# Kernel optimization log

Measured on AMD Instinct MI355X. Metric: run time of the kernel, lower is better.

## Reference

```python
import jax, jax.numpy as jnp
import numpy as np
from jax import lax

# module constants (from init_kwargs)
IN_CH = 128
OUT_CH = 128
CTX = 128
KS = 3
STRIDE = 1
PAD = 1
GROUPS = 1
ATT_GROUPS = 1
K = 4
TEMP = 30.0  # T_max, used as the fixed temperature at init


def setup_inputs() -> dict:
    key = jax.random.key(0)
    k1, k2, k3, k4, k5 = jax.random.split(key, 5)
    b, f, t = 16, 64, 256
    x = jax.random.normal(k1, (b, IN_CH, f, t), dtype=jnp.float32)
    g = jax.random.normal(k2, (1, b, CTX), dtype=jnp.float32)
    # Dense(k*att_groups) params (kaiming-normal kernel, zero bias)
    fan_in = CTX
    dense_kernel = jax.random.normal(k3, (CTX, K * ATT_GROUPS), dtype=jnp.float32) * np.sqrt(2.0 / fan_in)
    dense_bias = jnp.zeros((K * ATT_GROUPS,), dtype=jnp.float32)
    # kernel bank: (k, out, in//groups, ks, ks) -> swapaxes(1,2) -> flatten to (1, att_groups, k, -1)
    flat = OUT_CH * (IN_CH // GROUPS) * KS * KS // ATT_GROUPS
    weight = jax.random.normal(k4, (1, ATT_GROUPS, K, flat), dtype=jnp.float32) * np.sqrt(2.0 / flat)
    return {"x": x, "g": g, "dense_kernel": dense_kernel, "dense_bias": dense_bias, "weight": weight}


def reference(x, g, dense_kernel, dense_bias, weight):
    b, c, f, t = x.shape
    g_c = g[0].reshape(b, -1)                                  # [b, ctx]
    residuals = (g_c @ dense_kernel + dense_bias).reshape(b, ATT_GROUPS, 1, -1)  # [b, ag, 1, k]
    attention = jax.nn.softmax(residuals / TEMP, axis=-1)      # [b, ag, 1, k]
    # per-sample kernel aggregation: [b, ag, 1, k] @ [1, ag, k, D] -> [b, ag, 1, D]
    agg = (attention @ weight).swapaxes(1, 2)                  # [b, 1, ag, D]
    agg = agg.reshape(b * OUT_CH, IN_CH // GROUPS, KS, KS)
    # batch-as-groups grouped conv
    out = lax.conv_general_dilated(
        x.reshape(1, b * c, f, t), agg,
        window_strides=(STRIDE, STRIDE),
        padding=[(PAD, PAD), (PAD, PAD)],
        dimension_numbers=("NCHW", "OIHW", "NCHW"),
        feature_group_count=b * GROUPS,
    )
    return out.reshape(b, OUT_CH, out.shape[-2], out.shape[-1])
```

## Files before the change

kernel.cpp:

```cpp
#include <hip/hip_runtime.h>
#include <stdint.h>

#define NB 16
#define NC 128
#define NOC 128
#define NF 64
#define NT 256
#define NCTX 128
#define NTAPS 9
#define NFLAT 147456
#define TEMPR 30.0f

#define ICP 40
#define XCOLS 258
#define SX_ELEMS (3*XCOLS*ICP)
#define SW_ELEMS (NTAPS*NOC*ICP)

typedef float f32x4 __attribute__((ext_vector_type(4)));
typedef __bf16 bf16x8 __attribute__((ext_vector_type(8)));
typedef unsigned int u32x4 __attribute__((ext_vector_type(4)));

__device__ __forceinline__ unsigned short f2bf(float f) {
    union { float f; unsigned u; } v; v.f = f;
    unsigned r = v.u + 0x7fffu + ((v.u >> 16) & 1u);
    return (unsigned short)(r >> 16);
}

__global__ void attn_kernel(const float* __restrict__ g,
                            const float* __restrict__ dk,
                            const float* __restrict__ bias,
                            float* __restrict__ att) {
    int b = threadIdx.x;
    if (b >= NB) return;
    float r0 = bias[0], r1 = bias[1], r2 = bias[2], r3 = bias[3];
    const float* gb = g + b * NCTX;
    for (int c = 0; c < NCTX; ++c) {
        float gv = gb[c];
        r0 += gv * dk[c*4+0];
        r1 += gv * dk[c*4+1];
        r2 += gv * dk[c*4+2];
        r3 += gv * dk[c*4+3];
    }
    r0 *= (1.0f/TEMPR); r1 *= (1.0f/TEMPR); r2 *= (1.0f/TEMPR); r3 *= (1.0f/TEMPR);
    float mx = fmaxf(fmaxf(r0, r1), fmaxf(r2, r3));
    float e0 = expf(r0-mx), e1 = expf(r1-mx), e2 = expf(r2-mx), e3 = expf(r3-mx);
    float s = e0+e1+e2+e3;
    att[b*4+0] = e0/s; att[b*4+1] = e1/s; att[b*4+2] = e2/s; att[b*4+3] = e3/s;
}

__global__ void agg_kernel(const float* __restrict__ w,
                           const float* __restrict__ att,
                           unsigned short* __restrict__ wb) {
    int idx = blockIdx.x * 256 + threadIdx.x;
    int ic = idx & 127;
    int oc = (idx >> 7) & 127;
    int b  = idx >> 14;
    float a0 = att[b*4+0], a1 = att[b*4+1], a2 = att[b*4+2], a3 = att[b*4+3];
    int d0 = (oc*NC + ic) * NTAPS;
    #pragma unroll
    for (int tap = 0; tap < NTAPS; ++tap) {
        float s = a0 * w[0*NFLAT + d0 + tap]
                + a1 * w[1*NFLAT + d0 + tap]
                + a2 * w[2*NFLAT + d0 + tap]
                + a3 * w[3*NFLAT + d0 + tap];
        wb[((b*NTAPS + tap)*NOC + oc)*NC + ic] = f2bf(s);
    }
}

__global__ __launch_bounds__(512) void conv_kernel(
        const float* __restrict__ x,
        const unsigned short* __restrict__ wb,
        float* __restrict__ out) {
    __shared__ unsigned short sx[SX_ELEMS];
    __shared__ unsigned short sw[SW_ELEMS];

    const int p  = blockIdx.x;
    const int lg = (p & 7) * 128 + (p >> 3);
    const int b  = lg >> 6;
    const int y  = lg & 63;

    const int tid  = threadIdx.x;
    const int lane = tid & 63;
    const int wid  = tid >> 6;
    const int wpix = wid & 3;
    const int woc  = wid >> 2;
    const int l15  = lane & 15;
    const int l4   = lane >> 4;

    f32x4 acc[4][4];
    #pragma unroll
    for (int m = 0; m < 4; ++m)
        #pragma unroll
        for (int n = 0; n < 4; ++n)
            acc[m][n] = (f32x4){0.f, 0.f, 0.f, 0.f};

    const float* xb = x + (b * NC) * (NF * NT);
    const unsigned short* wbb = wb + b * (NTAPS * NOC * NC);

    for (int c4 = 0; c4 < 4; ++c4) {
        const int ic0 = c4 * 32;
        __syncthreads();

        #pragma unroll
        for (int j = 0; j < 6; ++j) {
            int w_  = tid + j * 512;
            int qlo = w_ & 3;
            int i2  = (w_ >> 2) & 15;
            int qhi = (w_ >> 6) & 15;
            int r   = w_ >> 10;
            int q   = qhi * 4 + qlo;
            int iy  = y - 1 + r;
            f32x4 v0 = (f32x4){0.f,0.f,0.f,0.f};
            f32x4 v1 = v0;
            if ((unsigned)iy < (unsigned)NF) {
                const float* src = xb + ((ic0 + 2*i2) * NF + iy) * NT + q * 4;
                v0 = *(const f32x4*)src;
                v1 = *(const f32x4*)(src + NF * NT);
            }
            unsigned short* dst = sx + (r * XCOLS + q*4 + 1) * ICP + 2*i2;
            #pragma unroll
            for (int jj = 0; jj < 4; ++jj) {
                unsigned pk = (unsigned)f2bf(v0[jj]) | ((unsigned)f2bf(v1[jj]) << 16);
                *(unsigned*)(dst + jj * ICP) = pk;
            }
        }
        if (tid < 96) {
            int i2 = tid & 15;
            int rr = tid >> 4;
            int r  = rr % 3;
            int c  = (rr / 3) ? (XCOLS - 1) : 0;
            *(unsigned*)(sx + (r * XCOLS + c) * ICP + 2*i2) = 0u;
        }

        #pragma unroll
        for (int j = 0; j < 9; ++j) {
            int w_  = tid + j * 512;
            int row = w_ >> 2;
            int q4  = w_ & 3;
            u32x4 d = *(const u32x4*)(wbb + row * NC + ic0 + q4 * 8);
            *(u32x4*)(sw + row * ICP + q4 * 8) = d;
        }
        __syncthreads();

        const unsigned short* swp = sw + (woc * 64 + l15) * ICP + l4 * 8;
        const unsigned short* sxp = sx + (wpix * 64 + l15) * ICP + l4 * 8;
        #pragma unroll
        for (int ky = 0; ky < 3; ++ky) {
            #pragma unroll
            for (int kx = 0; kx < 3; ++kx) {
                const int tap = ky * 3 + kx;
                bf16x8 af[4], bfv[4];
                #pragma unroll
                for (int m = 0; m < 4; ++m)
                    af[m] = *(const bf16x8*)(swp + (tap * NOC + m * 16) * ICP);
                #pragma unroll
                for (int n = 0; n < 4; ++n)
                    bfv[n] = *(const bf16x8*)(sxp + (ky * XCOLS + kx + n * 16) * ICP);
                #pragma unroll
                for (int m = 0; m < 4; ++m)
                    #pragma unroll
                    for (int n = 0; n < 4; ++n)
                        acc[m][n] = __builtin_amdgcn_mfma_f32_16x16x32_bf16(
                            af[m], bfv[n], acc[m][n], 0, 0, 0);
            }
        }
    }

    #pragma unroll
    for (int m = 0; m < 4; ++m) {
        int ocb = woc * 64 + m * 16 + l4 * 4;
        #pragma unroll
        for (int r = 0; r < 4; ++r) {
            float* orow = out + ((b * NOC + ocb + r) * NF + y) * NT;
            #pragma unroll
            for (int n = 0; n < 4; ++n)
                orow[wpix * 64 + n * 16 + l15] = acc[m][n][r];
        }
    }
}

extern "C" void kernel_launch(void* const* d_in, const int* in_sizes, int n_in,
                              void* d_out, int out_size, void* d_ws, size_t ws_size,
                              hipStream_t stream) {
    const float* x    = (const float*)d_in[0];
    const float* g    = (const float*)d_in[1];
    const float* dk   = (const float*)d_in[2];
    const float* bias = (const float*)d_in[3];
    const float* w    = (const float*)d_in[4];
    float* out = (float*)d_out;

    float* att = (float*)d_ws;
    unsigned short* wb = (unsigned short*)((char*)d_ws + 256);

    attn_kernel<<<dim3(1), dim3(64), 0, stream>>>(g, dk, bias, att);
    agg_kernel<<<dim3(1024), dim3(256), 0, stream>>>(w, att, wb);
    conv_kernel<<<dim3(1024), dim3(512), 0, stream>>>(x, wb, out);
}
```

Baseline: 127.5 us.

## Compute two output rows per block to reuse staged weights and halo rows

Each conv block now produces two output rows instead of one, staging four input rows and sharing the per-sample weight tile across both. The grid is halved and each wave holds a 4x8 accumulator tile covering half of one row. This cuts redundant weight and halo loads into LDS per output row. The LDS row padding shrinks from 40 to 36, launch bounds request two blocks per CU, and bf16 conversion switches to native casts. The larger accumulator raises register pressure, and the new padding may change bank-conflict behavior.

```diff
diff --git a/kernel.cpp b/kernel.cpp
--- a/kernel.cpp
+++ b/kernel.cpp
@@ -11,20 +11,16 @@
 #define NFLAT 147456
 #define TEMPR 30.0f
 
-#define ICP 40
+#define ICP 36
 #define XCOLS 258
-#define SX_ELEMS (3*XCOLS*ICP)
+#define XROWS 4
+#define SX_ELEMS (XROWS*XCOLS*ICP)
 #define SW_ELEMS (NTAPS*NOC*ICP)
 
 typedef float f32x4 __attribute__((ext_vector_type(4)));
 typedef __bf16 bf16x8 __attribute__((ext_vector_type(8)));
+typedef __bf16 bf16x2 __attribute__((ext_vector_type(2)));
 typedef unsigned int u32x4 __attribute__((ext_vector_type(4)));
-
-__device__ __forceinline__ unsigned short f2bf(float f) {
-    union { float f; unsigned u; } v; v.f = f;
-    unsigned r = v.u + 0x7fffu + ((v.u >> 16) & 1u);
-    return (unsigned short)(r >> 16);
-}
 
 __global__ void attn_kernel(const float* __restrict__ g,
                             const float* __restrict__ dk,
@@ -63,11 +59,13 @@
                 + a1 * w[1*NFLAT + d0 + tap]
                 + a2 * w[2*NFLAT + d0 + tap]
                 + a3 * w[3*NFLAT + d0 + tap];
-        wb[((b*NTAPS + tap)*NOC + oc)*NC + ic] = f2bf(s);
-    }
-}
-
-__global__ __launch_bounds__(512) void conv_kernel(
+        __bf16 h = (__bf16)s;
+        unsigned short u = *(unsigned short*)&h;
+        wb[((b*NTAPS + tap)*NOC + oc)*NC + ic] = u;
+    }
+}
+
+__global__ __launch_bounds__(512, 2) void conv_kernel(
         const float* __restrict__ x,
         const unsigned short* __restrict__ wb,
         float* __restrict__ out) {
@@ -75,9 +73,9 @@
     __shared__ unsigned short sw[SW_ELEMS];
 
     const int p  = blockIdx.x;
-    const int lg = (p & 7) * 128 + (p >> 3);
-    const int b  = lg >> 6;
-    const int y  = lg & 63;
+    const int lg = (p & 7) * 64 + (p >> 3);
+    const int b  = lg >> 5;
+    const int y0 = (lg & 31) * 2;
 
     const int tid  = threadIdx.x;
     const int lane = tid & 63;
@@ -87,29 +85,37 @@
     const int l15  = lane & 15;
     const int l4   = lane >> 4;
 
-    f32x4 acc[4][4];
+    f32x4 acc[4][8];
     #pragma unroll
     for (int m = 0; m < 4; ++m)
         #pragma unroll
-        for (int n = 0; n < 4; ++n)
+        for (int n = 0; n < 8; ++n)
             acc[m][n] = (f32x4){0.f, 0.f, 0.f, 0.f};
 
     const float* xb = x + (b * NC) * (NF * NT);
     const unsigned short* wbb = wb + b * (NTAPS * NOC * NC);
+
+    if (tid < 128) {
+        int i2 = tid & 15;
+        int rr = tid >> 4;
+        int r  = rr & 3;
+        int c  = (rr >> 2) ? (XCOLS - 1) : 0;
+        *(unsigned*)(sx + (r * XCOLS + c) * ICP + 2*i2) = 0u;
+    }
 
     for (int c4 = 0; c4 < 4; ++c4) {
         const int ic0 = c4 * 32;
         __syncthreads();
 
         #pragma unroll
-        for (int j = 0; j < 6; ++j) {
+        for (int j = 0; j < 8; ++j) {
             int w_  = tid + j * 512;
             int qlo = w_ & 3;
             int i2  = (w_ >> 2) & 15;
             int qhi = (w_ >> 6) & 15;
             int r   = w_ >> 10;
             int q   = qhi * 4 + qlo;
-            int iy  = y - 1 + r;
+            int iy  = y0 - 1 + r;
             f32x4 v0 = (f32x4){0.f,0.f,0.f,0.f};
             f32x4 v1 = v0;
             if ((unsigned)iy < (unsigned)NF) {
@@ -120,16 +126,11 @@
             unsigned short* dst = sx + (r * XCOLS + q*4 + 1) * ICP + 2*i2;
             #pragma unroll
             for (int jj = 0; jj < 4; ++jj) {
-                unsigned pk = (unsigned)f2bf(v0[jj]) | ((unsigned)f2bf(v1[jj]) << 16);
-                *(unsigned*)(dst + jj * ICP) = pk;
+                bf16x2 pk;
+                pk[0] = (__bf16)v0[jj];
+                pk[1] = (__bf16)v1[jj];
+                *(bf16x2*)(dst + jj * ICP) = pk;
             }
-        }
-        if (tid < 96) {
-            int i2 = tid & 15;
-            int rr = tid >> 4;
-            int r  = rr % 3;
-            int c  = (rr / 3) ? (XCOLS - 1) : 0;
-            *(unsigned*)(sx + (r * XCOLS + c) * ICP + 2*i2) = 0u;
         }
 
         #pragma unroll
@@ -143,38 +144,42 @@
         __syncthreads();
 
         const unsigned short* swp = sw + (woc * 64 + l15) * ICP + l4 * 8;
-        const unsigned short* sxp = sx + (wpix * 64 + l15) * ICP + l4 * 8;
+        const unsigned short* sxp = sx + l15 * ICP + l4 * 8;
+        const int yy    = wpix >> 1;
+        const int tbase = (wpix & 1) * 128;
         #pragma unroll
         for (int ky = 0; ky < 3; ++ky) {
             #pragma unroll
             for (int kx = 0; kx < 3; ++kx) {
                 const int tap = ky * 3 + kx;
-                bf16x8 af[4], bfv[4];
+                bf16x8 af[4], bfv[8];
                 #pragma unroll
                 for (int m = 0; m < 4; ++m)
                     af[m] = *(const bf16x8*)(swp + (tap * NOC + m * 16) * ICP);
                 #pragma unroll
-                for (int n = 0; n < 4; ++n)
-                    bfv[n] = *(const bf16x8*)(sxp + (ky * XCOLS + kx + n * 16) * ICP);
+                for (int n = 0; n < 8; ++n)
+                    bfv[n] = *(const bf16x8*)(sxp + ((yy + ky) * XCOLS + tbase + kx + n * 16) * ICP);
                 #pragma unroll
                 for (int m = 0; m < 4; ++m)
                     #pragma unroll
-                    for (int n = 0; n < 4; ++n)
+                    for (int n = 0; n < 8; ++n)
                         acc[m][n] = __builtin_amdgcn_mfma_f32_16x16x32_bf16(
                             af[m], bfv[n], acc[m][n], 0, 0, 0);
             }
         }
     }
 
+    const int yy    = wpix >> 1;
+    const int tbase = (wpix & 1) * 128;
     #pragma unroll
     for (int m = 0; m < 4; ++m) {
         int ocb = woc * 64 + m * 16 + l4 * 4;
         #pragma unroll
         for (int r = 0; r < 4; ++r) {
-            float* orow = out + ((b * NOC + ocb + r) * NF + y) * NT;
+            float* orow = out + ((b * NOC + ocb + r) * NF + (y0 + yy)) * NT;
             #pragma unroll
-            for (int n = 0; n < 4; ++n)
-                orow[wpix * 64 + n * 16 + l15] = acc[m][n][r];
+            for (int n = 0; n < 8; ++n)
+                orow[tbase + n * 16 + l15] = acc[m][n][r];
         }
     }
 }
@@ -194,5 +199,5 @@
 
     attn_kernel<<<dim3(1), dim3(64), 0, stream>>>(g, dk, bias, att);
     agg_kernel<<<dim3(1024), dim3(256), 0, stream>>>(w, att, wb);
-    conv_kernel<<<dim3(1024), dim3(512), 0, stream>>>(x, wb, out);
-}
+    conv_kernel<<<dim3(512), dim3(512), 0, stream>>>(x, wb, out);
+}
```

Result: slower. 260.6 us (+104.3%).

## Prefetch conv weight slices into registers and shrink LDS row padding

Applied to the files above, without the earlier changes.

The conv kernel now loads each 32-channel weight slice from global memory into registers while the MFMA loop for the previous slice runs, then writes it to LDS after the barrier. This is meant to hide global load latency. The zeroing of the padded border columns is moved out of the channel loop, and float-to-bf16 conversion uses native __bf16 casts instead of manual rounding. LDS row padding drops from 40 to 36 elements, which cuts LDS use but makes the row stride 72 bytes. That breaks 16-byte alignment for the vector LDS accesses and may change bank-conflict behaviour.

```diff
diff --git a/kernel.cpp b/kernel.cpp
--- a/kernel.cpp
+++ b/kernel.cpp
@@ -11,20 +11,16 @@
 #define NFLAT 147456
 #define TEMPR 30.0f
 
-#define ICP 40
+#define ICP 36
 #define XCOLS 258
-#define SX_ELEMS (3*XCOLS*ICP)
+#define XROWS 3
+#define SX_ELEMS (XROWS*XCOLS*ICP)
 #define SW_ELEMS (NTAPS*NOC*ICP)
 
 typedef float f32x4 __attribute__((ext_vector_type(4)));
 typedef __bf16 bf16x8 __attribute__((ext_vector_type(8)));
+typedef __bf16 bf16x2 __attribute__((ext_vector_type(2)));
 typedef unsigned int u32x4 __attribute__((ext_vector_type(4)));
-
-__device__ __forceinline__ unsigned short f2bf(float f) {
-    union { float f; unsigned u; } v; v.f = f;
-    unsigned r = v.u + 0x7fffu + ((v.u >> 16) & 1u);
-    return (unsigned short)(r >> 16);
-}
 
 __global__ void attn_kernel(const float* __restrict__ g,
                             const float* __restrict__ dk,
@@ -63,7 +59,9 @@
                 + a1 * w[1*NFLAT + d0 + tap]
                 + a2 * w[2*NFLAT + d0 + tap]
                 + a3 * w[3*NFLAT + d0 + tap];
-        wb[((b*NTAPS + tap)*NOC + oc)*NC + ic] = f2bf(s);
+        __bf16 h = (__bf16)s;
+        unsigned short u = *(unsigned short*)&h;
+        wb[((b*NTAPS + tap)*NOC + oc)*NC + ic] = u;
     }
 }
 
@@ -97,9 +95,34 @@
     const float* xb = x + (b * NC) * (NF * NT);
     const unsigned short* wbb = wb + b * (NTAPS * NOC * NC);
 
+    if (tid < 96) {
+        int i2 = tid & 15;
+        int rr = tid >> 4;
+        int r  = rr % 3;
+        int c  = (rr / 3) ? (XCOLS - 1) : 0;
+        *(unsigned*)(sx + (r * XCOLS + c) * ICP + 2*i2) = 0u;
+    }
+
+    const unsigned short* const swp = sw + (woc * 64 + l15) * ICP + l4 * 8;
+    const unsigned short* const sxp = sx + (wpix * 64 + l15) * ICP + l4 * 8;
+
+    const int wrow = tid >> 2;
+    const int wq4  = tid & 3;
+    const unsigned short* const wsrc = wbb + wrow * NC + wq4 * 8;
+    unsigned short* const wdst = sw + wrow * ICP + wq4 * 8;
+
+    u32x4 wreg[9];
+    #pragma unroll
+    for (int j = 0; j < 9; ++j)
+        wreg[j] = *(const u32x4*)(wsrc + j * 128 * NC);
+
     for (int c4 = 0; c4 < 4; ++c4) {
         const int ic0 = c4 * 32;
         __syncthreads();
+
+        #pragma unroll
+        for (int j = 0; j < 9; ++j)
+            *(u32x4*)(wdst + j * 128 * ICP) = wreg[j];
 
         #pragma unroll
         for (int j = 0; j < 6; ++j) {
@@ -120,30 +143,20 @@
             unsigned short* dst = sx + (r * XCOLS + q*4 + 1) * ICP + 2*i2;
             #pragma unroll
             for (int jj = 0; jj < 4; ++jj) {
-                unsigned pk = (unsigned)f2bf(v0[jj]) | ((unsigned)f2bf(v1[jj]) << 16);
-                *(unsigned*)(dst + jj * ICP) = pk;
+                bf16x2 pk;
+                pk[0] = (__bf16)v0[jj];
+                pk[1] = (__bf16)v1[jj];
+                *(bf16x2*)(dst + jj * ICP) = pk;
             }
         }
-        if (tid < 96) {
-            int i2 = tid & 15;
-            int rr = tid >> 4;
-            int r  = rr % 3;
-            int c  = (rr / 3) ? (XCOLS - 1) : 0;
-            *(unsigned*)(sx + (r * XCOLS + c) * ICP + 2*i2) = 0u;
-        }
-
-        #pragma unroll
-        for (int j = 0; j < 9; ++j) {
-            int w_  = tid + j * 512;
-            int row = w_ >> 2;
-            int q4  = w_ & 3;
-            u32x4 d = *(const u32x4*)(wbb + row * NC + ic0 + q4 * 8);
-            *(u32x4*)(sw + row * ICP + q4 * 8) = d;
-        }
         __syncthreads();
 
-        const unsigned short* swp = sw + (woc * 64 + l15) * ICP + l4 * 8;
-        const unsigned short* sxp = sx + (wpix * 64 + l15) * ICP + l4 * 8;
+        if (c4 < 3) {
+            #pragma unroll
+            for (int j = 0; j < 9; ++j)
+                wreg[j] = *(const u32x4*)(wsrc + j * 128 * NC + (ic0 + 32));
+        }
+
         #pragma unroll
         for (int ky = 0; ky < 3; ++ky) {
             #pragma unroll
```

Measured after the change: 344.7 us. 170% more time.

## Reorganize LDS and weight buffers into 8-element chunk layout, hoist halo zeroing

Applied to the files above, without the earlier changes.

Shared-memory tiles for x and weights switch from padded rows (ICP=40) to a chunked layout where each 16-byte k-chunk of a pixel or output channel is contiguous across pixels. The aggregation kernel writes weights directly in this chunked order, so each block copies its weight slice with plain contiguous loads. Halo-column zeroing moves out of the channel loop, and manual bf16 rounding is replaced by native __bf16 casts. The aim is fewer LDS bank conflicts on the MFMA operand reads, a smaller LDS footprint and cheaper staging, at the risk of new conflicts on the scattered x-tile stores.

```diff
diff --git a/kernel.cpp b/kernel.cpp
--- a/kernel.cpp
+++ b/kernel.cpp
@@ -11,20 +11,14 @@
 #define NFLAT 147456
 #define TEMPR 30.0f
 
-#define ICP 40
 #define XCOLS 258
-#define SX_ELEMS (3*XCOLS*ICP)
-#define SW_ELEMS (NTAPS*NOC*ICP)
+#define XROWS 3
+#define SX_CHUNKS (XROWS*4*XCOLS)
+#define SW_CHUNKS (NTAPS*4*NOC)
 
 typedef float f32x4 __attribute__((ext_vector_type(4)));
 typedef __bf16 bf16x8 __attribute__((ext_vector_type(8)));
 typedef unsigned int u32x4 __attribute__((ext_vector_type(4)));
-
-__device__ __forceinline__ unsigned short f2bf(float f) {
-    union { float f; unsigned u; } v; v.f = f;
-    unsigned r = v.u + 0x7fffu + ((v.u >> 16) & 1u);
-    return (unsigned short)(r >> 16);
-}
 
 __global__ void attn_kernel(const float* __restrict__ g,
                             const float* __restrict__ dk,
@@ -57,13 +51,19 @@
     int b  = idx >> 14;
     float a0 = att[b*4+0], a1 = att[b*4+1], a2 = att[b*4+2], a3 = att[b*4+3];
     int d0 = (oc*NC + ic) * NTAPS;
+    int c4 = ic >> 5;
+    int kq = (ic >> 3) & 3;
+    int e  = ic & 7;
     #pragma unroll
     for (int tap = 0; tap < NTAPS; ++tap) {
         float s = a0 * w[0*NFLAT + d0 + tap]
                 + a1 * w[1*NFLAT + d0 + tap]
                 + a2 * w[2*NFLAT + d0 + tap]
                 + a3 * w[3*NFLAT + d0 + tap];
-        wb[((b*NTAPS + tap)*NOC + oc)*NC + ic] = f2bf(s);
+        __bf16 h = (__bf16)s;
+        unsigned short u = *(unsigned short*)&h;
+        int chunk = (tap * 4 + kq) * 128 + oc;
+        wb[(((b * 4 + c4) * (NTAPS*4*NOC)) + chunk) * 8 + e] = u;
     }
 }
 
@@ -71,8 +71,8 @@
         const float* __restrict__ x,
         const unsigned short* __restrict__ wb,
         float* __restrict__ out) {
-    __shared__ unsigned short sx[SX_ELEMS];
-    __shared__ unsigned short sw[SW_ELEMS];
+    __shared__ unsigned short sx[SX_CHUNKS * 8];
+    __shared__ unsigned short sw[SW_CHUNKS * 8];
 
     const int p  = blockIdx.x;
     const int lg = (p & 7) * 128 + (p >> 3);
@@ -96,6 +96,19 @@
 
     const float* xb = x + (b * NC) * (NF * NT);
     const unsigned short* wbb = wb + b * (NTAPS * NOC * NC);
+
+    if (tid < 96) {
+        int piece = tid & 3;
+        int gch   = tid >> 2;
+        int r     = gch / 8;
+        int rem   = gch & 7;
+        int kq    = rem >> 1;
+        int c     = (rem & 1) ? (XCOLS - 1) : 0;
+        *(unsigned*)(sx + (((r * 4 + kq) * XCOLS + c) * 8) + piece * 2) = 0u;
+    }
+
+    const unsigned short* const swp = sw + (l4 * NOC + woc * 64 + l15) * 8;
+    const unsigned short* const sxp = sx + (l4 * XCOLS + wpix * 64 + l15) * 8;
 
     for (int c4 = 0; c4 < 4; ++c4) {
         const int ic0 = c4 * 32;
@@ -117,33 +130,28 @@
                 v0 = *(const f32x4*)src;
                 v1 = *(const f32x4*)(src + NF * NT);
             }
-            unsigned short* dst = sx + (r * XCOLS + q*4 + 1) * ICP + 2*i2;
+            const int kq = i2 >> 2;
+            const int e0 = (2 * i2) & 7;
+            unsigned short* dst = sx + ((r * 4 + kq) * XCOLS + q * 4 + 1) * 8 + e0;
             #pragma unroll
             for (int jj = 0; jj < 4; ++jj) {
-                unsigned pk = (unsigned)f2bf(v0[jj]) | ((unsigned)f2bf(v1[jj]) << 16);
-                *(unsigned*)(dst + jj * ICP) = pk;
+                __bf16 h0 = (__bf16)v0[jj];
+                __bf16 h1 = (__bf16)v1[jj];
+                unsigned pk = (unsigned)*(unsigned short*)&h0
+                            | ((unsigned)*(unsigned short*)&h1 << 16);
+                *(unsigned*)(dst + jj * 8) = pk;
             }
         }
-        if (tid < 96) {
-            int i2 = tid & 15;
-            int rr = tid >> 4;
-            int r  = rr % 3;
-            int c  = (rr / 3) ? (XCOLS - 1) : 0;
-            *(unsigned*)(sx + (r * XCOLS + c) * ICP + 2*i2) = 0u;
-        }
-
+
+        const unsigned short* wsrc = wbb + c4 * (SW_CHUNKS * 8);
         #pragma unroll
         for (int j = 0; j < 9; ++j) {
-            int w_  = tid + j * 512;
-            int row = w_ >> 2;
-            int q4  = w_ & 3;
-            u32x4 d = *(const u32x4*)(wbb + row * NC + ic0 + q4 * 8);
-            *(u32x4*)(sw + row * ICP + q4 * 8) = d;
+            int chunk = tid + j * 512;
+            u32x4 d = *(const u32x4*)(wsrc + chunk * 8);
+            *(u32x4*)(sw + chunk * 8) = d;
         }
         __syncthreads();
 
-        const unsigned short* swp = sw + (woc * 64 + l15) * ICP + l4 * 8;
-        const unsigned short* sxp = sx + (wpix * 64 + l15) * ICP + l4 * 8;
         #pragma unroll
         for (int ky = 0; ky < 3; ++ky) {
             #pragma unroll
@@ -152,10 +160,10 @@
                 bf16x8 af[4], bfv[4];
                 #pragma unroll
                 for (int m = 0; m < 4; ++m)
-                    af[m] = *(const bf16x8*)(swp + (tap * NOC + m * 16) * ICP);
+                    af[m] = *(const bf16x8*)(swp + (tap * 4 * NOC + m * 16) * 8);
                 #pragma unroll
                 for (int n = 0; n < 4; ++n)
-                    bfv[n] = *(const bf16x8*)(sxp + (ky * XCOLS + kx + n * 16) * ICP);
+                    bfv[n] = *(const bf16x8*)(sxp + (ky * 4 * XCOLS + kx + n * 16) * 8);
                 #pragma unroll
                 for (int m = 0; m < 4; ++m)
                     #pragma unroll
```

New measurement: 124.5 us. -2.3%, faster.
